# Performance work log

Hardware: AMD Instinct MI355X
Metric: run time of the kernel (lower is better)

The kernel has to match this reference:

```python
import jax, jax.numpy as jnp
import numpy as np

HID = 64
HEADS = 4


def setup_inputs() -> dict:
    key = jax.random.key(0)
    ks = jax.random.split(key, 16)
    B, N = 128, 8192
    s = lambda *shape: 0.05  # init scale
    inp = {
        "radar_xy": jax.random.normal(ks[0], (B, 2), jnp.float32),
        "radar_dir": jax.random.normal(ks[1], (B, 2), jnp.float32),
        "pts": jax.random.normal(ks[2], (B, N, 2), jnp.float32),
        # point_encoder: Linear(6,64) -> ReLU -> Linear(64,64)
        "enc_w1": jax.random.normal(ks[3], (6, HID), jnp.float32) * 0.4,
        "enc_b1": jnp.zeros((HID,), jnp.float32),
        "enc_w2": jax.random.normal(ks[4], (HID, HID), jnp.float32) * 0.125,
        "enc_b2": jnp.zeros((HID,), jnp.float32),
        # per-head score nets: Linear(6,64) -> ReLU -> Linear(64,1), stacked over heads
        "sc_w1": jax.random.normal(ks[5], (HEADS, 6, HID), jnp.float32) * 0.4,
        "sc_b1": jnp.zeros((HEADS, HID), jnp.float32),
        "sc_w2": jax.random.normal(ks[6], (HEADS, HID), jnp.float32) * 0.125,
        "sc_b2": jnp.zeros((HEADS,), jnp.float32),
        # output_mlp: Linear(64*4, 64) -> ReLU -> Linear(64, 1)
        "out_w1": jax.random.normal(ks[7], (HID * HEADS, 64), jnp.float32) * 0.0625,
        "out_b1": jnp.zeros((64,), jnp.float32),
        "out_w2": jax.random.normal(ks[8], (64, 1), jnp.float32) * 0.125,
        "out_b2": jnp.zeros((1,), jnp.float32),
    }
    return inp


def reference(radar_xy, radar_dir, pts,
              enc_w1, enc_b1, enc_w2, enc_b2,
              sc_w1, sc_b1, sc_w2, sc_b2,
              out_w1, out_b1, out_w2, out_b2):
    B, N, _ = pts.shape
    radar = jnp.concatenate([radar_xy, radar_dir], axis=-1)            # [B,4]
    radar = jnp.broadcast_to(radar[:, None, :], (B, N, 4))
    pairwise = jnp.concatenate([radar, pts], axis=-1)                  # [B,N,6]

    # point encoder: [B,N,6] -> [B,N,HID]
    h = jax.nn.relu(pairwise @ enc_w1 + enc_b1)
    point_features = h @ enc_w2 + enc_b2                               # [B,N,HID]

    # all heads at once: logits [B,N,HEADS]
    sh = jax.nn.relu(jnp.einsum('bnf,hfd->bnhd', pairwise, sc_w1) + sc_b1)
    logits = jnp.einsum('bnhd,hd->bnh', sh, sc_w2) + sc_b2             # [B,N,H]
    weights = jax.nn.softmax(logits, axis=1)                           # softmax over N

    # weighted pooling per head then concat (head-major, matching torch cat order)
    contexts = jnp.einsum('bnh,bnd->bhd', weights, point_features)     # [B,H,HID]
    full_context = contexts.reshape(B, HEADS * HID)

    o = jax.nn.relu(full_context @ out_w1 + out_b1)
    out = (o @ out_w2 + out_b2).squeeze(-1)                            # [B]
    return out
```

## Files before the change

kernel.cpp:

```cpp
#include <hip/hip_runtime.h>

#define HID 64
#define HEADS 4
#define TPB 256
#define PPT 8
#define BLK_PTS (TPB * PPT)

static __device__ __forceinline__ float rdl(float v, int l) {
    return __int_as_float(__builtin_amdgcn_readlane(__float_as_int(v), l));
}

__global__ __launch_bounds__(TPB) void k_main(
    const float* __restrict__ rxy, const float* __restrict__ rdir,
    const float* __restrict__ pts,
    const float* __restrict__ ew1, const float* __restrict__ eb1,
    const float* __restrict__ sw1, const float* __restrict__ sb1,
    const float* __restrict__ sw2,
    float* __restrict__ Ug, float* __restrict__ Tg, int N)
{
    __shared__ float4 spack[HEADS * HID];
    const int tid = threadIdx.x;
    const int b = blockIdx.y;
    const float rx = rxy[2 * b], ry = rxy[2 * b + 1];
    const float dx = rdir[2 * b], dy = rdir[2 * b + 1];

    {
        const int h = tid >> 6, d = tid & 63;
        const float* w = sw1 + (h * 6) * HID + d;
        float base = sb1[tid];
        base = fmaf(rx, w[0 * HID], base);
        base = fmaf(ry, w[1 * HID], base);
        base = fmaf(dx, w[2 * HID], base);
        base = fmaf(dy, w[3 * HID], base);
        spack[tid] = make_float4(base, w[4 * HID], w[5 * HID], sw2[tid]);
    }
    __syncthreads();

    const int lane = tid & 63;
    float baseE = eb1[lane];
    baseE = fmaf(rx, ew1[0 * HID + lane], baseE);
    baseE = fmaf(ry, ew1[1 * HID + lane], baseE);
    baseE = fmaf(dx, ew1[2 * HID + lane], baseE);
    baseE = fmaf(dy, ew1[3 * HID + lane], baseE);
    const float wxE = ew1[4 * HID + lane];
    const float wyE = ew1[5 * HID + lane];

    const int wave = tid >> 6;
    const int wbase = blockIdx.x * BLK_PTS + wave * (64 * PPT);
    const float2* __restrict__ p2 = reinterpret_cast<const float2*>(pts) + (size_t)b * N;

    float px[PPT], py[PPT];
#pragma unroll
    for (int j = 0; j < PPT; ++j) {
        const int n = wbase + j * 64 + lane;
        const int nc = (n < N) ? n : (N - 1);
        const float2 p = p2[nc];
        px[j] = p.x; py[j] = p.y;
    }

    float a0[PPT], a1[PPT], a2[PPT], a3[PPT];
#pragma unroll
    for (int j = 0; j < PPT; ++j) { a0[j] = 0.f; a1[j] = 0.f; a2[j] = 0.f; a3[j] = 0.f; }

#define SCORE_H(ACC, H)                                                     \
    _Pragma("unroll 4")                                                     \
    for (int d = 0; d < HID; ++d) {                                         \
        const float4 wp = spack[(H) * HID + d];                             \
        _Pragma("unroll")                                                   \
        for (int j = 0; j < PPT; ++j) {                                     \
            const float s = fmaf(py[j], wp.z, fmaf(px[j], wp.y, wp.x));     \
            ACC[j] = fmaf(fmaxf(s, 0.f), wp.w, ACC[j]);                     \
        }                                                                   \
    }
    SCORE_H(a0, 0)
    SCORE_H(a1, 1)
    SCORE_H(a2, 2)
    SCORE_H(a3, 3)
#undef SCORE_H

    float T0 = 0.f, T1 = 0.f, T2 = 0.f, T3 = 0.f;
#pragma unroll
    for (int j = 0; j < PPT; ++j) {
        const bool v = (wbase + j * 64 + lane) < N;
        a0[j] = v ? __expf(a0[j]) : 0.f;
        a1[j] = v ? __expf(a1[j]) : 0.f;
        a2[j] = v ? __expf(a2[j]) : 0.f;
        a3[j] = v ? __expf(a3[j]) : 0.f;
        T0 += a0[j]; T1 += a1[j]; T2 += a2[j]; T3 += a3[j];
    }

    float U0 = 0.f, U1 = 0.f, U2 = 0.f, U3 = 0.f;
    for (int p = 0; p < 64; ++p) {
#pragma unroll
        for (int j = 0; j < PPT; ++j) {
            const float spx = rdl(px[j], p);
            const float spy = rdl(py[j], p);
            float hv = fmaf(spy, wyE, fmaf(spx, wxE, baseE));
            hv = fmaxf(hv, 0.f);
            U0 = fmaf(rdl(a0[j], p), hv, U0);
            U1 = fmaf(rdl(a1[j], p), hv, U1);
            U2 = fmaf(rdl(a2[j], p), hv, U2);
            U3 = fmaf(rdl(a3[j], p), hv, U3);
        }
    }

#pragma unroll
    for (int off = 32; off; off >>= 1) {
        T0 += __shfl_xor(T0, off);
        T1 += __shfl_xor(T1, off);
        T2 += __shfl_xor(T2, off);
        T3 += __shfl_xor(T3, off);
    }

    float* __restrict__ Ub = Ug + (size_t)b * (HEADS * HID);
    atomicAdd(&Ub[0 * HID + lane], U0);
    atomicAdd(&Ub[1 * HID + lane], U1);
    atomicAdd(&Ub[2 * HID + lane], U2);
    atomicAdd(&Ub[3 * HID + lane], U3);
    if (lane == 0) {
        float* __restrict__ Tb = Tg + (size_t)b * HEADS;
        atomicAdd(&Tb[0], T0);
        atomicAdd(&Tb[1], T1);
        atomicAdd(&Tb[2], T2);
        atomicAdd(&Tb[3], T3);
    }
}

__global__ __launch_bounds__(64) void k_final(
    const float* __restrict__ Ug, const float* __restrict__ Tg,
    const float* __restrict__ ew2, const float* __restrict__ eb2,
    const float* __restrict__ ow1, const float* __restrict__ ob1,
    const float* __restrict__ ow2, const float* __restrict__ ob2,
    float* __restrict__ out)
{
    const int b = blockIdx.x;
    const int d = threadIdx.x;
    const float* __restrict__ Ub = Ug + (size_t)b * (HEADS * HID);
    const float iT0 = 1.f / Tg[b * 4 + 0];
    const float iT1 = 1.f / Tg[b * 4 + 1];
    const float iT2 = 1.f / Tg[b * 4 + 2];
    const float iT3 = 1.f / Tg[b * 4 + 3];

    float c0 = 0.f, c1 = 0.f, c2 = 0.f, c3 = 0.f;
#pragma unroll 8
    for (int k = 0; k < HID; ++k) {
        const float w2kd = ew2[k * HID + d];
        c0 = fmaf(Ub[0 * HID + k], w2kd, c0);
        c1 = fmaf(Ub[1 * HID + k], w2kd, c1);
        c2 = fmaf(Ub[2 * HID + k], w2kd, c2);
        c3 = fmaf(Ub[3 * HID + k], w2kd, c3);
    }
    const float e2 = eb2[d];
    const float fc0 = fmaf(c0, iT0, e2);
    const float fc1 = fmaf(c1, iT1, e2);
    const float fc2 = fmaf(c2, iT2, e2);
    const float fc3 = fmaf(c3, iT3, e2);

    float o = ob1[d];
#pragma unroll 4
    for (int k = 0; k < 64; ++k) {
        o = fmaf(rdl(fc0, k), ow1[(0 * 64 + k) * 64 + d], o);
        o = fmaf(rdl(fc1, k), ow1[(1 * 64 + k) * 64 + d], o);
        o = fmaf(rdl(fc2, k), ow1[(2 * 64 + k) * 64 + d], o);
        o = fmaf(rdl(fc3, k), ow1[(3 * 64 + k) * 64 + d], o);
    }
    o = fmaxf(o, 0.f) * ow2[d];
#pragma unroll
    for (int off = 32; off; off >>= 1) o += __shfl_xor(o, off);
    if (d == 0) out[b] = o + ob2[0];
}

extern "C" void kernel_launch(void* const* d_in, const int* in_sizes, int n_in,
                              void* d_out, int out_size, void* d_ws, size_t ws_size,
                              hipStream_t stream)
{
    const float* rxy  = (const float*)d_in[0];
    const float* rdir = (const float*)d_in[1];
    const float* pts  = (const float*)d_in[2];
    const float* ew1  = (const float*)d_in[3];
    const float* eb1  = (const float*)d_in[4];
    const float* ew2  = (const float*)d_in[5];
    const float* eb2  = (const float*)d_in[6];
    const float* sw1  = (const float*)d_in[7];
    const float* sb1  = (const float*)d_in[8];
    const float* sw2  = (const float*)d_in[9];
    const float* ow1  = (const float*)d_in[11];
    const float* ob1  = (const float*)d_in[12];
    const float* ow2  = (const float*)d_in[13];
    const float* ob2  = (const float*)d_in[14];
    float* out = (float*)d_out;

    const int B = in_sizes[0] / 2;
    const int N = in_sizes[2] / (2 * B);

    float* Ug = (float*)d_ws;
    float* Tg = Ug + (size_t)B * (HEADS * HID);
    hipMemsetAsync(Ug, 0, (size_t)B * (HEADS * HID + HEADS) * sizeof(float), stream);

    const int chunks = (N + BLK_PTS - 1) / BLK_PTS;
    k_main<<<dim3(chunks, B), TPB, 0, stream>>>(rxy, rdir, pts, ew1, eb1,
                                                sw1, sb1, sw2, Ug, Tg, N);
    k_final<<<dim3(B), 64, 0, stream>>>(Ug, Tg, ew2, eb2, ow1, ob1, ow2, ob2, out);
}
```

Baseline: 159.2 us.

## Rewrite score ReLU as abs identity, halve points per thread, widen final kernel

Uses relu(s) = 0.5*(s + |s|) so the score inner loop does an abs-fma, with the linear half precomputed per head as a wave-reduced constant that seeds the accumulators. Points per thread drop from 8 to 4, doubling the grid in the point dimension. The final kernel is split across 256 threads (one wave per head) with shared-memory partial sums instead of one wave looping over all heads. The identity is exact apart from rounding, but the smaller per-thread tile doubles the per-block setup and atomic traffic.

```diff
diff --git a/kernel.cpp b/kernel.cpp
--- a/kernel.cpp
+++ b/kernel.cpp
@@ -3,7 +3,7 @@
 #define HID 64
 #define HEADS 4
 #define TPB 256
-#define PPT 8
+#define PPT 4
 #define BLK_PTS (TPB * PPT)
 
 static __device__ __forceinline__ float rdl(float v, int l) {
@@ -19,20 +19,31 @@
     float* __restrict__ Ug, float* __restrict__ Tg, int N)
 {
     __shared__ float4 spack[HEADS * HID];
+    __shared__ float4 Ch[HEADS];
     const int tid = threadIdx.x;
     const int b = blockIdx.y;
     const float rx = rxy[2 * b], ry = rxy[2 * b + 1];
     const float dx = rdir[2 * b], dy = rdir[2 * b + 1];
 
     {
-        const int h = tid >> 6, d = tid & 63;
-        const float* w = sw1 + (h * 6) * HID + d;
+        const int h = tid >> 6;
+        const float* w = sw1 + (h * 6) * HID + (tid & 63);
         float base = sb1[tid];
         base = fmaf(rx, w[0 * HID], base);
         base = fmaf(ry, w[1 * HID], base);
         base = fmaf(dx, w[2 * HID], base);
         base = fmaf(dy, w[3 * HID], base);
-        spack[tid] = make_float4(base, w[4 * HID], w[5 * HID], sw2[tid]);
+        const float wx = w[4 * HID], wy = w[5 * HID];
+        const float w2h = 0.5f * sw2[tid];
+        spack[tid] = make_float4(base, wx, wy, w2h);
+        float c0 = w2h * base, c1 = w2h * wx, c2 = w2h * wy;
+#pragma unroll
+        for (int off = 32; off; off >>= 1) {
+            c0 += __shfl_xor(c0, off);
+            c1 += __shfl_xor(c1, off);
+            c2 += __shfl_xor(c2, off);
+        }
+        if ((tid & 63) == 0) Ch[h] = make_float4(c0, c1, c2, 0.f);
     }
     __syncthreads();
 
@@ -49,6 +60,8 @@
     const int wbase = blockIdx.x * BLK_PTS + wave * (64 * PPT);
     const float2* __restrict__ p2 = reinterpret_cast<const float2*>(pts) + (size_t)b * N;
 
+    const float4 CA = Ch[0], CB = Ch[1], CC = Ch[2], CD = Ch[3];
+
     float px[PPT], py[PPT];
 #pragma unroll
     for (int j = 0; j < PPT; ++j) {
@@ -60,7 +73,12 @@
 
     float a0[PPT], a1[PPT], a2[PPT], a3[PPT];
 #pragma unroll
-    for (int j = 0; j < PPT; ++j) { a0[j] = 0.f; a1[j] = 0.f; a2[j] = 0.f; a3[j] = 0.f; }
+    for (int j = 0; j < PPT; ++j) {
+        a0[j] = fmaf(py[j], CA.z, fmaf(px[j], CA.y, CA.x));
+        a1[j] = fmaf(py[j], CB.z, fmaf(px[j], CB.y, CB.x));
+        a2[j] = fmaf(py[j], CC.z, fmaf(px[j], CC.y, CC.x));
+        a3[j] = fmaf(py[j], CD.z, fmaf(px[j], CD.y, CD.x));
+    }
 
 #define SCORE_H(ACC, H)                                                     \
     _Pragma("unroll 4")                                                     \
@@ -69,7 +87,7 @@
         _Pragma("unroll")                                                   \
         for (int j = 0; j < PPT; ++j) {                                     \
             const float s = fmaf(py[j], wp.z, fmaf(px[j], wp.y, wp.x));     \
-            ACC[j] = fmaf(fmaxf(s, 0.f), wp.w, ACC[j]);                     \
+            ACC[j] = fmaf(__builtin_fabsf(s), wp.w, ACC[j]);                \
         }                                                                   \
     }
     SCORE_H(a0, 0)
@@ -126,7 +144,7 @@
     }
 }
 
-__global__ __launch_bounds__(64) void k_final(
+__global__ __launch_bounds__(256) void k_final(
     const float* __restrict__ Ug, const float* __restrict__ Tg,
     const float* __restrict__ ew2, const float* __restrict__ eb2,
     const float* __restrict__ ow1, const float* __restrict__ ob1,
@@ -134,40 +152,35 @@
     float* __restrict__ out)
 {
     const int b = blockIdx.x;
-    const int d = threadIdx.x;
-    const float* __restrict__ Ub = Ug + (size_t)b * (HEADS * HID);
-    const float iT0 = 1.f / Tg[b * 4 + 0];
-    const float iT1 = 1.f / Tg[b * 4 + 1];
-    const float iT2 = 1.f / Tg[b * 4 + 2];
-    const float iT3 = 1.f / Tg[b * 4 + 3];
-
-    float c0 = 0.f, c1 = 0.f, c2 = 0.f, c3 = 0.f;
+    const int t = threadIdx.x;
+    const int h = t >> 6, d = t & 63;
+    __shared__ float fcs[HEADS * HID];
+    __shared__ float partials[256];
+
+    const float* __restrict__ Ub = Ug + (size_t)b * (HEADS * HID) + h * HID;
+    const float iT = 1.f / Tg[b * HEADS + h];
+    float acc = 0.f;
 #pragma unroll 8
-    for (int k = 0; k < HID; ++k) {
-        const float w2kd = ew2[k * HID + d];
-        c0 = fmaf(Ub[0 * HID + k], w2kd, c0);
-        c1 = fmaf(Ub[1 * HID + k], w2kd, c1);
-        c2 = fmaf(Ub[2 * HID + k], w2kd, c2);
-        c3 = fmaf(Ub[3 * HID + k], w2kd, c3);
-    }
-    const float e2 = eb2[d];
-    const float fc0 = fmaf(c0, iT0, e2);
-    const float fc1 = fmaf(c1, iT1, e2);
-    const float fc2 = fmaf(c2, iT2, e2);
-    const float fc3 = fmaf(c3, iT3, e2);
-
-    float o = ob1[d];
-#pragma unroll 4
-    for (int k = 0; k < 64; ++k) {
-        o = fmaf(rdl(fc0, k), ow1[(0 * 64 + k) * 64 + d], o);
-        o = fmaf(rdl(fc1, k), ow1[(1 * 64 + k) * 64 + d], o);
-        o = fmaf(rdl(fc2, k), ow1[(2 * 64 + k) * 64 + d], o);
-        o = fmaf(rdl(fc3, k), ow1[(3 * 64 + k) * 64 + d], o);
-    }
-    o = fmaxf(o, 0.f) * ow2[d];
-#pragma unroll
-    for (int off = 32; off; off >>= 1) o += __shfl_xor(o, off);
-    if (d == 0) out[b] = o + ob2[0];
+    for (int k = 0; k < HID; ++k)
+        acc = fmaf(Ub[k], ew2[k * HID + d], acc);
+    fcs[t] = fmaf(acc, iT, eb2[d]);
+    __syncthreads();
+
+    float part = (h == 0) ? ob1[d] : 0.f;
+    const float* __restrict__ fq = fcs + h * HID;
+#pragma unroll 8
+    for (int k = 0; k < HID; ++k)
+        part = fmaf(fq[k], ow1[(h * HID + k) * 64 + d], part);
+    partials[t] = part;
+    __syncthreads();
+
+    if (t < 64) {
+        float o = partials[t] + partials[t + 64] + partials[t + 128] + partials[t + 192];
+        o = fmaxf(o, 0.f) * ow2[t];
+#pragma unroll
+        for (int off = 32; off; off >>= 1) o += __shfl_xor(o, off);
+        if (t == 0) out[b] = o + ob2[0];
+    }
 }
 
 extern "C" void kernel_launch(void* const* d_in, const int* in_sizes, int n_in,
@@ -200,5 +213,5 @@
     const int chunks = (N + BLK_PTS - 1) / BLK_PTS;
     k_main<<<dim3(chunks, B), TPB, 0, stream>>>(rxy, rdir, pts, ew1, eb1,
                                                 sw1, sb1, sw2, Ug, Tg, N);
-    k_final<<<dim3(B), 64, 0, stream>>>(Ug, Tg, ew2, eb2, ow1, ob1, ow2, ob2, out);
-}
+    k_final<<<dim3(B), 256, 0, stream>>>(Ug, Tg, ew2, eb2, ow1, ob1, ow2, ob2, out);
+}
```

After: 158.1 us. About the same (-0.7%).
